# Kernel optimization log

Hardware: AMD Instinct MI355X
Metric: run time of the kernel (lower is better)

Reference implementation:

```python
import jax, jax.numpy as jnp
import numpy as np

B, N, E, T, DIN, H, G, ND, NT, L = 4, 10000, 320000, 16, 16, 64, 64, 16, 3, 7


def _mlp2(x, W1, b1, W2, b2):
    # Linear -> LeakyReLU -> (Dropout: eval identity) -> Linear -> LeakyReLU
    h = jax.nn.leaky_relu(x @ W1 + b1)
    return jax.nn.leaky_relu(h @ W2 + b2)


def _gcn_conv(x, src, dst, ew, nt, W1, b1, W2, b2):
    # x: [B,N,D], nt: [B,N,ND], ew: [*,E,1] broadcastable over batch
    x_in = _mlp2(jnp.concatenate([x, nt], axis=-1), W1, b1, W2, b2)  # [B,N,G]
    msgs = x_in[:, src, :] * ew                                      # gather + weight, [B,E,G]
    aggr = jnp.zeros(x_in.shape, x_in.dtype).at[:, dst, :].add(msgs) # scatter-add, [B,N,G]
    return x + aggr


def _gru(x, Wx, Wh, bx, bh):
    # PyTorch-style GRU over time axis. x: [B,N,T,DIN] -> hs: [T,B,N,H]
    xw = jnp.einsum('bntd,dh->tbnh', x, Wx) + bx  # precompute input projections [T,B,N,3H]
    h0 = jnp.zeros(x.shape[:2] + (Wh.shape[0],), x.dtype)

    def step(h, xw_t):
        hw = h @ Wh + bh
        xr, xz, xn = jnp.split(xw_t, 3, axis=-1)
        hr, hz, hn = jnp.split(hw, 3, axis=-1)
        r = jax.nn.sigmoid(xr + hr)
        z = jax.nn.sigmoid(xz + hz)
        n = jnp.tanh(xn + r * hn)
        h_new = (1 - z) * n + z * h
        return h_new, h_new

    _, hs = jax.lax.scan(step, h0, xw)
    return hs


def reference(input_day, edge_attr, gru_Wx, gru_Wh, gru_bx, gru_bh,
              rnn_fc_W, rnn_fc_b,
              e_emb, e_c0_W1, e_c0_b1, e_c0_W2, e_c0_b2,
              e_c1_W1, e_c1_b1, e_c1_W2, e_c1_b2,
              e_fm_W1, e_fm_b1, e_fm_W2, e_fm_b2,
              g_emb, g_c0_W1, g_c0_b1, g_c0_W2, g_c0_b2,
              g_c1_W1, g_c1_b1, g_c1_W2, g_c1_b2,
              gcn_fc_W, gcn_fc_b,
              edge_index, node_type_ids):
    src, dst = edge_index[0], edge_index[1]

    # KRNN encoder (GRU) + max over time + FC head
    hs = _gru(input_day, gru_Wx, gru_Wh, gru_bx, gru_bh)  # [T,B,N,H]
    rnn_out = hs.max(axis=0)                              # kr_out.max(dim=-2) -> [B,N,H]
    y_rnn = rnn_out @ rnn_fc_W + rnn_fc_b                 # [B,N,L]

    # EdgeNet: GCN stack on static edge_attr, then per-edge pair MLP -> gate
    nt_e = jnp.broadcast_to(e_emb[node_type_ids][None], (B, N, ND))
    ew0 = edge_attr.reshape(1, E, 1)
    x = rnn_out
    x = _gcn_conv(x, src, dst, ew0, nt_e, e_c0_W1, e_c0_b1, e_c0_W2, e_c0_b2)
    x = _gcn_conv(x, src, dst, ew0, nt_e, e_c1_W1, e_c1_b1, e_c1_W2, e_c1_b2)
    edge_x = jnp.concatenate([x[:, src, :], x[:, dst, :]], axis=-1)  # [B,E,2G]
    h = jax.nn.leaky_relu(edge_x @ e_fm_W1 + e_fm_b1)
    edge_gate = jax.nn.relu(h @ e_fm_W2 + e_fm_b2)                   # [B,E,1]

    # Main GCNNet with learned edge gates
    nt_g = jnp.broadcast_to(g_emb[node_type_ids][None], (B, N, ND))
    x = rnn_out
    x = _gcn_conv(x, src, dst, edge_gate, nt_g, g_c0_W1, g_c0_b1, g_c0_W2, g_c0_b2)
    x = _gcn_conv(x, src, dst, edge_gate, nt_g, g_c1_W1, g_c1_b1, g_c1_W2, g_c1_b2)
    y_gcn = x @ gcn_fc_W + gcn_fc_b                                  # [B,N,L]

    return y_rnn + y_gcn


def setup_inputs() -> dict:
    key = jax.random.key(0)
    ks = iter(jax.random.split(key, 48))

    def nrm(shape, s=0.1):
        return jax.random.normal(next(ks), shape, jnp.float32) * s

    inp = {}
    inp['input_day'] = jax.random.normal(next(ks), (B, N, T, DIN), jnp.float32)
    inp['edge_index'] = jax.random.randint(next(ks), (2, E), 0, N)
    inp['node_type_ids'] = jax.random.randint(next(ks), (N,), 0, NT)
    inp['edge_attr'] = jax.random.uniform(next(ks), (E,), jnp.float32)

    inp['gru_Wx'] = nrm((DIN, 3 * H))
    inp['gru_Wh'] = nrm((H, 3 * H))
    inp['gru_bx'] = jnp.zeros((3 * H,), jnp.float32)
    inp['gru_bh'] = jnp.zeros((3 * H,), jnp.float32)
    inp['rnn_fc_W'] = nrm((H, L))
    inp['rnn_fc_b'] = jnp.zeros((L,), jnp.float32)

    inp['e_emb'] = nrm((NT, ND))
    inp['g_emb'] = nrm((NT, ND))
    for pre, in_dim in (('e_c0', H + ND), ('e_c1', G + ND), ('g_c0', H + ND), ('g_c1', G + ND)):
        inp[pre + '_W1'] = nrm((in_dim, G))
        inp[pre + '_b1'] = jnp.zeros((G,), jnp.float32)
        inp[pre + '_W2'] = nrm((G, G))
        inp[pre + '_b2'] = jnp.zeros((G,), jnp.float32)

    inp['e_fm_W1'] = nrm((2 * G, G))
    inp['e_fm_b1'] = jnp.zeros((G,), jnp.float32)
    inp['e_fm_W2'] = nrm((G, 1))
    inp['e_fm_b2'] = jnp.zeros((1,), jnp.float32)

    inp['gcn_fc_W'] = nrm((G, L))
    inp['gcn_fc_b'] = jnp.zeros((L,), jnp.float32)
    return inp
```

## Files before the change

### kernel.cpp

```cpp
#include <hip/hip_runtime.h>
#include <hip/hip_bf16.h>

#define NB 4
#define NN 10000
#define NE 320000
#define BN 40000
#define NL 7

typedef float f32x4 __attribute__((ext_vector_type(4)));
typedef __bf16 bf16x8 __attribute__((ext_vector_type(8)));

__device__ __forceinline__ float bf2f(unsigned short u){
  unsigned x = ((unsigned)u) << 16;
  return __builtin_bit_cast(float, x);
}
__device__ __forceinline__ unsigned short f2bf(float f){
  unsigned u = __builtin_bit_cast(unsigned, f);
  u += 0x7fffu + ((u >> 16) & 1u);
  return (unsigned short)(u >> 16);
}
__device__ __forceinline__ __bf16 f2b(float f){
  return __builtin_bit_cast(__bf16, f2bf(f));
}
__device__ __forceinline__ bf16x8 zero8(){
  uint4 z = make_uint4(0u,0u,0u,0u);
  return __builtin_bit_cast(bf16x8, z);
}
__device__ __forceinline__ bf16x8 one8(){
  uint4 z = make_uint4(0x3f80u,0u,0u,0u);
  return __builtin_bit_cast(bf16x8, z);
}
__device__ __forceinline__ bf16x8 ld8bf(const unsigned short* p){
  uint4 u = *(const uint4*)p;
  return __builtin_bit_cast(bf16x8, u);
}
__device__ __forceinline__ unsigned pk2(float lo, float hi){
  unsigned r;
  asm("v_cvt_pk_bf16_f32 %0, %1, %2" : "=v"(r) : "v"(lo), "v"(hi));
  return r;
}
__device__ __forceinline__ bf16x8 ld8f(const float* p){
  float4 a = *(const float4*)p;
  float4 b = *(const float4*)(p+4);
  uint4 u = make_uint4(pk2(a.x,a.y), pk2(a.z,a.w), pk2(b.x,b.y), pk2(b.z,b.w));
  return __builtin_bit_cast(bf16x8, u);
}
__device__ __forceinline__ float frcp(float x){ return __builtin_amdgcn_rcpf(x); }
__device__ __forceinline__ float sigm(float x){ return frcp(1.f+__expf(-x)); }
__device__ __forceinline__ float tanh_(float x){ return 1.f - 2.f*frcp(__expf(2.f*x)+1.f); }
__device__ __forceinline__ float lrelu(float x){ return x > 0.f ? x : 0.01f*x; }

#define LDS_WAIT() asm volatile("s_waitcnt lgkmcnt(0)" ::: "memory")

__global__ __launch_bounds__(256, 2) void gru_kernel(
    const float* __restrict__ xd,
    const float* __restrict__ Wx,
    const float* __restrict__ Wh,
    const float* __restrict__ bx,
    const float* __restrict__ bh,
    float* __restrict__ rnn)
{
  __shared__ __attribute__((aligned(16))) unsigned short WhT[192][72];
  __shared__ __attribute__((aligned(16))) unsigned short WxT[192][40];
  __shared__ __attribute__((aligned(16))) unsigned short hb[4][16][72];
  int tid = threadIdx.x;
  int wave = tid >> 6, lane = tid & 63;
  int ln16 = lane & 15, quad = lane >> 4;

  for (int i = tid; i < 64*192; i += 256){
    int k = i / 192, n = i - k*192;
    WhT[n][k] = f2bf(Wh[i]);
  }
  for (int i = tid; i < 16*192; i += 256){
    int k = i / 192, n = i - k*192;
    WxT[n][k] = f2bf(Wx[i]);
    WxT[n][17+k] = 0;
  }
  if (tid < 192){
    float bias = (tid < 128) ? (bx[tid] + bh[tid]) : bx[tid];
    WxT[tid][16] = f2bf(bias);
  }
  for (int i = tid; i < 4*16*72; i += 256) ((unsigned short*)hb)[i] = 0;
  __syncthreads();

  int rowbase = blockIdx.x * 64 + wave * 16;

  bf16x8 whf[2][12];
  #pragma unroll
  for (int kt=0; kt<2; ++kt)
    #pragma unroll
    for (int nt=0; nt<12; ++nt)
      whf[kt][nt] = ld8bf(&WhT[nt*16 + ln16][kt*32 + quad*8]);

  f32x4 bhn2[4];
  #pragma unroll
  for (int j=0;j<4;++j)
    bhn2[j] = *(const f32x4*)(bh + 128 + j*16 + quad*4);

  f32x4 hprev[4], vmax[4];
  #pragma unroll
  for (int j=0;j<4;++j){
    hprev[j] = (f32x4){0.f,0.f,0.f,0.f};
    vmax[j]  = (f32x4){-1e30f,-1e30f,-1e30f,-1e30f};
  }

  const float* xrow = xd + (size_t)(rowbase + ln16) * 256;
  unsigned short* hrow = &hb[wave][ln16][0];

  bf16x8 axc;
  if (quad < 2) axc = ld8f(xrow + quad*8);
  else          axc = (quad == 2) ? one8() : zero8();

  for (int t = 0; t < 16; ++t){
    bf16x8 axn;
    if (quad < 2) axn = (t < 15) ? ld8f(xrow + (t+1)*16 + quad*8) : zero8();
    else          axn = (quad == 2) ? one8() : zero8();
    bf16x8 ah0 = ld8bf(hrow + quad*8);
    bf16x8 ah1 = ld8bf(hrow + 32 + quad*8);

    #pragma unroll
    for (int j=0;j<4;++j){
      bf16x8 xr = ld8bf(&WxT[j*16+ln16][quad*8]);
      bf16x8 xz = ld8bf(&WxT[(4+j)*16+ln16][quad*8]);
      bf16x8 xn = ld8bf(&WxT[(8+j)*16+ln16][quad*8]);
      f32x4 z4 = (f32x4){0.f,0.f,0.f,0.f};
      f32x4 ar = __builtin_amdgcn_mfma_f32_16x16x32_bf16(xr, axc, z4, 0,0,0);
      ar = __builtin_amdgcn_mfma_f32_16x16x32_bf16(whf[0][j], ah0, ar, 0,0,0);
      ar = __builtin_amdgcn_mfma_f32_16x16x32_bf16(whf[1][j], ah1, ar, 0,0,0);
      f32x4 az = __builtin_amdgcn_mfma_f32_16x16x32_bf16(xz, axc, z4, 0,0,0);
      az = __builtin_amdgcn_mfma_f32_16x16x32_bf16(whf[0][4+j], ah0, az, 0,0,0);
      az = __builtin_amdgcn_mfma_f32_16x16x32_bf16(whf[1][4+j], ah1, az, 0,0,0);
      f32x4 an = __builtin_amdgcn_mfma_f32_16x16x32_bf16(xn, axc, z4, 0,0,0);
      f32x4 ah = __builtin_amdgcn_mfma_f32_16x16x32_bf16(whf[0][8+j], ah0, bhn2[j], 0,0,0);
      ah = __builtin_amdgcn_mfma_f32_16x16x32_bf16(whf[1][8+j], ah1, ah, 0,0,0);
      f32x4 hv;
      #pragma unroll
      for (int i=0;i<4;++i){
        float r  = sigm(ar[i]);
        float z  = sigm(az[i]);
        float nn = tanh_(an[i] + r * ah[i]);
        float h  = fmaf(z, hprev[j][i]-nn, nn);
        hprev[j][i] = h;
        vmax[j][i] = fmaxf(vmax[j][i], h);
        hv[i] = h;
      }
      *(uint2*)&hb[wave][ln16][j*16+quad*4] = make_uint2(pk2(hv[0],hv[1]), pk2(hv[2],hv[3]));
    }
    LDS_WAIT();
    axc = axn;
  }
  float* orow = rnn + (size_t)(rowbase + ln16)*64;
  #pragma unroll
  for (int j=0;j<4;++j)
    *(f32x4*)(orow + j*16 + quad*4) = vmax[j];
}

__global__ __launch_bounds__(256, 2) void mlp2_kernel(
    const float* __restrict__ x,
    const int* __restrict__ ntid,
    const float* __restrict__ emb,
    const float* __restrict__ W1,
    const float* __restrict__ b1,
    const float* __restrict__ W2,
    const float* __restrict__ b2,
    unsigned short* __restrict__ out)
{
  __shared__ __attribute__((aligned(16))) unsigned short W1T[64][96];
  __shared__ __attribute__((aligned(16))) unsigned short W2T[64][72];
  __shared__ __attribute__((aligned(16))) unsigned short hb[4][16][72];
  __shared__ float sb1[64], sb2[64];
  int tid = threadIdx.x;
  for (int i=tid;i<80*64;i+=256){ int k=i>>6, n=i&63; W1T[n][k]=f2bf(W1[i]); }
  for (int i=tid;i<64*16;i+=256){ int n=i>>4, k=80+(i&15); W1T[n][k]=0; }
  for (int i=tid;i<64*64;i+=256){ int k=i>>6, n=i&63; W2T[n][k]=f2bf(W2[i]); }
  if (tid<64){ sb1[tid]=b1[tid]; sb2[tid]=b2[tid]; }
  __syncthreads();

  int wave = tid>>6, lane = tid&63, ln16 = lane&15, quad = lane>>4;
  int row0 = blockIdx.x*64 + wave*16;
  int r_ = row0 + ln16;
  const float* xr = x + (size_t)r_*64;
  bf16x8 a0 = ld8f(xr + quad*8);
  bf16x8 a1 = ld8f(xr + 32 + quad*8);
  int id = ntid[r_ % NN];
  bf16x8 a2 = (quad<2) ? ld8f(emb + id*16 + quad*8) : zero8();

  f32x4 acc[4];
  #pragma unroll
  for (int nt=0;nt<4;++nt){
    float bb = sb1[nt*16+ln16];
    acc[nt] = (f32x4){bb,bb,bb,bb};
    acc[nt] = __builtin_amdgcn_mfma_f32_16x16x32_bf16(a0, ld8bf(&W1T[nt*16+ln16][quad*8]),    acc[nt], 0,0,0);
    acc[nt] = __builtin_amdgcn_mfma_f32_16x16x32_bf16(a1, ld8bf(&W1T[nt*16+ln16][32+quad*8]), acc[nt], 0,0,0);
    acc[nt] = __builtin_amdgcn_mfma_f32_16x16x32_bf16(a2, ld8bf(&W1T[nt*16+ln16][64+quad*8]), acc[nt], 0,0,0);
  }
  #pragma unroll
  for (int nt=0;nt<4;++nt)
    #pragma unroll
    for (int i=0;i<4;++i)
      hb[wave][quad*4+i][nt*16+ln16] = f2bf(lrelu(acc[nt][i]));
  LDS_WAIT();
  bf16x8 h0 = ld8bf(&hb[wave][ln16][quad*8]);
  bf16x8 h1 = ld8bf(&hb[wave][ln16][32+quad*8]);
  f32x4 acc2[4];
  #pragma unroll
  for (int nt=0;nt<4;++nt){
    float bb = sb2[nt*16+ln16];
    acc2[nt] = (f32x4){bb,bb,bb,bb};
    acc2[nt] = __builtin_amdgcn_mfma_f32_16x16x32_bf16(h0, ld8bf(&W2T[nt*16+ln16][quad*8]),    acc2[nt], 0,0,0);
    acc2[nt] = __builtin_amdgcn_mfma_f32_16x16x32_bf16(h1, ld8bf(&W2T[nt*16+ln16][32+quad*8]), acc2[nt], 0,0,0);
  }
  #pragma unroll
  for (int nt=0;nt<4;++nt)
    #pragma unroll
    for (int i=0;i<4;++i)
      out[(size_t)(row0+quad*4+i)*64 + nt*16+ln16] = f2bf(lrelu(acc2[nt][i]));
}

__global__ __launch_bounds__(256, 2) void uv_kernel(
    const float* __restrict__ x,
    const float* __restrict__ W1,
    unsigned short* __restrict__ uvp)
{
  __shared__ __attribute__((aligned(16))) unsigned short WT[128][72];
  int tid=threadIdx.x;
  for (int i=tid;i<64*64;i+=256){
    int k=i>>6, n=i&63;
    WT[n][k]    = f2bf(W1[i]);
    WT[64+n][k] = f2bf(W1[64*64 + i]);
  }
  __syncthreads();
  int wave=tid>>6, lane=tid&63, ln16=lane&15, quad=lane>>4;
  int row0 = blockIdx.x*64 + wave*16;
  const float* xr = x + (size_t)(row0+ln16)*64;
  bf16x8 a0 = ld8f(xr + quad*8);
  bf16x8 a1 = ld8f(xr + 32 + quad*8);
  f32x4 acc[8];
  #pragma unroll
  for (int nt=0;nt<8;++nt){
    acc[nt] = (f32x4){0.f,0.f,0.f,0.f};
    acc[nt] = __builtin_amdgcn_mfma_f32_16x16x32_bf16(a0, ld8bf(&WT[nt*16+ln16][quad*8]),    acc[nt], 0,0,0);
    acc[nt] = __builtin_amdgcn_mfma_f32_16x16x32_bf16(a1, ld8bf(&WT[nt*16+ln16][32+quad*8]), acc[nt], 0,0,0);
  }
  #pragma unroll
  for (int nt=0;nt<8;++nt)
    #pragma unroll
    for (int i=0;i<4;++i)
      uvp[(size_t)(row0+quad*4+i)*128 + nt*16+ln16] = f2bf(acc[nt][i]);
}

__global__ __launch_bounds__(256) void count_kernel(const int* __restrict__ ei, int* __restrict__ counts){
  int e = blockIdx.x*256+threadIdx.x;
  atomicAdd(&counts[ei[NE+e]], 1);
}
__global__ __launch_bounds__(1024) void scan_kernel(const int* __restrict__ counts,
                                                    int* __restrict__ rowptr, int* __restrict__ cursor){
  __shared__ int incl[10240];
  __shared__ int wsum[16];
  int tid=threadIdx.x, wave=tid>>6, lane=tid&63;
  int base = wave*640;
  int carry=0;
  #pragma unroll
  for (int c=0;c<10;++c){
    int i = base + c*64 + lane;
    int v = (i<NN)? counts[i] : 0;
    int s = v;
    #pragma unroll
    for (int off=1;off<64;off<<=1){
      int t_ = __shfl_up(s, off);
      if (lane>=off) s += t_;
    }
    s += carry;
    incl[base + c*64 + lane] = s;
    carry = __shfl(s, 63);
  }
  if (lane==63) wsum[wave]=carry;
  __syncthreads();
  if (wave==0){
    int w_ = (lane<16)? wsum[lane]:0;
    #pragma unroll
    for (int off=1;off<16;off<<=1){
      int t_ = __shfl_up(w_, off);
      if (lane>=off) w_ += t_;
    }
    if (lane<16) wsum[lane]=w_;
  }
  __syncthreads();
  int woff = (wave>0)? wsum[wave-1] : 0;
  #pragma unroll
  for (int c=0;c<10;++c){
    int i = base + c*64 + lane;
    if (i<NN){
      int excl = incl[i] + woff - counts[i];
      rowptr[i]=excl; cursor[i]=excl;
    }
  }
  if (tid==0) rowptr[NN]=wsum[15];
}
__global__ __launch_bounds__(256) void fill_kernel(const int* __restrict__ ei,
                                                   const float* __restrict__ ea,
                                                   int* __restrict__ cursor,
                                                   int* __restrict__ ssrc,
                                                   float* __restrict__ wcsr){
  int e = blockIdx.x*256+threadIdx.x;
  int d = ei[NE+e];
  int pos = atomicAdd(&cursor[d],1);
  ssrc[pos]=ei[e];
  wcsr[pos]=ea[e];
}

__global__ __launch_bounds__(256) void aggr_kernel(
    const float* x,
    const unsigned short* __restrict__ xin,
    const int* __restrict__ rowptr,
    const int* __restrict__ ssrc,
    const float* __restrict__ wp,
    int bstride,
    float* out)
{
  int tid=threadIdx.x;
  int wave=tid>>6, lane=tid&63;
  int sub=lane>>4, l=lane&15;
  int bid = blockIdx.x*4 + wave;
  int b = bid / NN, n = bid - b*NN;
  int p0 = rowptr[n], p1 = rowptr[n+1];
  const unsigned short* xb_ = xin + (size_t)b*NN*64;
  const float* wb = wp + (size_t)b*bstride;
  float a0=0.f, a1=0.f, a2=0.f, a3=0.f;
  #pragma unroll 4
  for (int p=p0+sub; p<p1; p+=4){
    int s = ssrc[p];
    float w = wb[p];
    uint2 m = *(const uint2*)(xb_ + (size_t)s*64 + l*4);
    a0 += bf2f((unsigned short)(m.x & 0xffffu)) * w;
    a1 += bf2f((unsigned short)(m.x >> 16)) * w;
    a2 += bf2f((unsigned short)(m.y & 0xffffu)) * w;
    a3 += bf2f((unsigned short)(m.y >> 16)) * w;
  }
  a0 += __shfl_xor(a0,16); a0 += __shfl_xor(a0,32);
  a1 += __shfl_xor(a1,16); a1 += __shfl_xor(a1,32);
  a2 += __shfl_xor(a2,16); a2 += __shfl_xor(a2,32);
  a3 += __shfl_xor(a3,16); a3 += __shfl_xor(a3,32);
  if (sub==0){
    float4 base = *(const float4*)(x + (size_t)bid*64 + l*4);
    float4 o; o.x=base.x+a0; o.y=base.y+a1; o.z=base.z+a2; o.w=base.w+a3;
    *(float4*)(out + (size_t)bid*64 + l*4) = o;
  }
}

__global__ __launch_bounds__(256) void aggr_final_kernel(
    const float* x,
    const unsigned short* __restrict__ xin,
    const int* __restrict__ rowptr,
    const int* __restrict__ ssrc,
    const float* __restrict__ wp,
    const float* __restrict__ rnn,
    const float* __restrict__ Wr, const float* __restrict__ br,
    const float* __restrict__ Wg, const float* __restrict__ bg,
    float* __restrict__ out)
{
  __shared__ float sWr[448], sWg[448], sb[7];
  int tid=threadIdx.x;
  for (int i=tid;i<448;i+=256){ sWr[i]=Wr[i]; sWg[i]=Wg[i]; }
  if (tid<7) sb[tid]=br[tid]+bg[tid];
  __syncthreads();
  int wave=tid>>6, lane=tid&63;
  int sub=lane>>4, l=lane&15;
  int bid = blockIdx.x*4 + wave;
  int b = bid / NN, n = bid - b*NN;
  int p0 = rowptr[n], p1 = rowptr[n+1];
  const unsigned short* xb_ = xin + (size_t)b*NN*64;
  const float* wb = wp + (size_t)b*NE;
  float a0=0.f, a1=0.f, a2=0.f, a3=0.f;
  #pragma unroll 4
  for (int p=p0+sub; p<p1; p+=4){
    int s = ssrc[p];
    float w = wb[p];
    uint2 m = *(const uint2*)(xb_ + (size_t)s*64 + l*4);
    a0 += bf2f((unsigned short)(m.x & 0xffffu)) * w;
    a1 += bf2f((unsigned short)(m.x >> 16)) * w;
    a2 += bf2f((unsigned short)(m.y & 0xffffu)) * w;
    a3 += bf2f((unsigned short)(m.y >> 16)) * w;
  }
  a0 += __shfl_xor(a0,16); a0 += __shfl_xor(a0,32);
  a1 += __shfl_xor(a1,16); a1 += __shfl_xor(a1,32);
  a2 += __shfl_xor(a2,16); a2 += __shfl_xor(a2,32);
  a3 += __shfl_xor(a3,16); a3 += __shfl_xor(a3,32);
  if (sub==0){
    float4 base = *(const float4*)(x + (size_t)bid*64 + l*4);
    float o0=base.x+a0, o1=base.y+a1, o2=base.z+a2, o3=base.w+a3;
    float4 rr = *(const float4*)(rnn + (size_t)bid*64 + l*4);
    float part[7];
    #pragma unroll
    for (int q=0;q<7;++q)
      part[q] = o0*sWg[(l*4+0)*7+q] + o1*sWg[(l*4+1)*7+q]
              + o2*sWg[(l*4+2)*7+q] + o3*sWg[(l*4+3)*7+q]
              + rr.x*sWr[(l*4+0)*7+q] + rr.y*sWr[(l*4+1)*7+q]
              + rr.z*sWr[(l*4+2)*7+q] + rr.w*sWr[(l*4+3)*7+q];
    #pragma unroll
    for (int q=0;q<7;++q){
      part[q] += __shfl_xor(part[q],1);
      part[q] += __shfl_xor(part[q],2);
      part[q] += __shfl_xor(part[q],4);
      part[q] += __shfl_xor(part[q],8);
    }
    if (l==0){
      #pragma unroll
      for (int q=0;q<7;++q) out[(size_t)bid*7+q] = part[q] + sb[q];
    }
  }
}

__global__ __launch_bounds__(256) void gate_kernel(
    const unsigned short* __restrict__ uvp,
    const int* __restrict__ rowptr,
    const int* __restrict__ ssrc,
    const float* __restrict__ b1,
    const float* __restrict__ W2,
    const float* __restrict__ b2,
    float* __restrict__ gate)
{
  int tid=threadIdx.x;
  int wave=tid>>6, lane=tid&63;
  int sub=lane>>4, l=lane&15;
  int bid = blockIdx.x*4 + wave;
  int b = bid / NN, n = bid - b*NN;
  int p0 = rowptr[n], p1 = rowptr[n+1];
  const unsigned short* ub = uvp + (size_t)b*NN*128;
  uint2 vu = *(const uint2*)(ub + (size_t)n*128 + 64 + l*4);
  float v0=bf2f((unsigned short)(vu.x&0xffffu)), v1=bf2f((unsigned short)(vu.x>>16));
  float v2=bf2f((unsigned short)(vu.y&0xffffu)), v3=bf2f((unsigned short)(vu.y>>16));
  float4 bb = *(const float4*)(b1 + l*4);
  float4 ww = *(const float4*)(W2 + l*4);
  float b2v = b2[0];
  float* gb = gate + (size_t)b*NE;
  #pragma unroll 4
  for (int p=p0+sub; p<p1; p+=4){
    int s = ssrc[p];
    uint2 uu = *(const uint2*)(ub + (size_t)s*128 + l*4);
    float h0 = lrelu(bf2f((unsigned short)(uu.x&0xffffu)) + v0 + bb.x);
    float h1 = lrelu(bf2f((unsigned short)(uu.x>>16))     + v1 + bb.y);
    float h2 = lrelu(bf2f((unsigned short)(uu.y&0xffffu)) + v2 + bb.z);
    float h3 = lrelu(bf2f((unsigned short)(uu.y>>16))     + v3 + bb.w);
    float part = h0*ww.x + h1*ww.y + h2*ww.z + h3*ww.w;
    part += __shfl_xor(part,1);
    part += __shfl_xor(part,2);
    part += __shfl_xor(part,4);
    part += __shfl_xor(part,8);
    if (l==0){
      float g = part + b2v;
      gb[p] = g>0.f ? g : 0.f;
    }
  }
}

extern "C" void kernel_launch(void* const* d_in, const int* in_sizes, int n_in,
                              void* d_out, int out_size, void* d_ws, size_t ws_size,
                              hipStream_t stream)
{
  (void)in_sizes; (void)n_in; (void)out_size; (void)ws_size;
  const float* input_day = (const float*)d_in[0];
  const int* ei    = (const int*)d_in[1];
  const int* ntid  = (const int*)d_in[2];
  const float* edge_attr = (const float*)d_in[3];
  const float* gWx = (const float*)d_in[4];
  const float* gWh = (const float*)d_in[5];
  const float* gbx = (const float*)d_in[6];
  const float* gbh = (const float*)d_in[7];
  const float* rW  = (const float*)d_in[8];
  const float* rb  = (const float*)d_in[9];
  const float* eemb= (const float*)d_in[10];
  const float* gemb= (const float*)d_in[11];
  const float* ec0W1=(const float*)d_in[12];
  const float* ec0b1=(const float*)d_in[13];
  const float* ec0W2=(const float*)d_in[14];
  const float* ec0b2=(const float*)d_in[15];
  const float* ec1W1=(const float*)d_in[16];
  const float* ec1b1=(const float*)d_in[17];
  const float* ec1W2=(const float*)d_in[18];
  const float* ec1b2=(const float*)d_in[19];
  const float* gc0W1=(const float*)d_in[20];
  const float* gc0b1=(const float*)d_in[21];
  const float* gc0W2=(const float*)d_in[22];
  const float* gc0b2=(const float*)d_in[23];
  const float* gc1W1=(const float*)d_in[24];
  const float* gc1b1=(const float*)d_in[25];
  const float* gc1W2=(const float*)d_in[26];
  const float* gc1b2=(const float*)d_in[27];
  const float* efmW1=(const float*)d_in[28];
  const float* efmb1=(const float*)d_in[29];
  const float* efmW2=(const float*)d_in[30];
  const float* efmb2=(const float*)d_in[31];
  const float* gcnW =(const float*)d_in[32];
  const float* gcnb =(const float*)d_in[33];

  char* ws = (char*)d_ws;
  float*          rnn = (float*)(ws);
  float*          xe  = (float*)(ws + 10240000);
  unsigned short* xin = (unsigned short*)(ws + 20480000);
  unsigned short* uvp = (unsigned short*)(ws + 25600000);
  float*          gat = (float*)(ws + 35840000);
  int* rowptr= (int*)(ws + 40960000);
  int* cursor= (int*)(ws + 41000064);
  int* counts= (int*)(ws + 41040064);
  int*   ssrc= (int*)(ws + 41080064);
  float* wcsr= (float*)(ws + 42360064);

  hipMemsetAsync(counts, 0, NN*sizeof(int), stream);
  count_kernel<<<NE/256, 256, 0, stream>>>(ei, counts);
  scan_kernel<<<1, 1024, 0, stream>>>(counts, rowptr, cursor);
  fill_kernel<<<NE/256, 256, 0, stream>>>(ei, edge_attr, cursor, ssrc, wcsr);

  gru_kernel<<<625, 256, 0, stream>>>(input_day, gWx, gWh, gbx, gbh, rnn);

  mlp2_kernel<<<625, 256, 0, stream>>>(rnn, ntid, eemb, ec0W1, ec0b1, ec0W2, ec0b2, xin);
  aggr_kernel<<<BN/4, 256, 0, stream>>>(rnn, xin, rowptr, ssrc, wcsr, 0, xe);
  mlp2_kernel<<<625, 256, 0, stream>>>(xe, ntid, eemb, ec1W1, ec1b1, ec1W2, ec1b2, xin);
  aggr_kernel<<<BN/4, 256, 0, stream>>>(xe, xin, rowptr, ssrc, wcsr, 0, xe);

  uv_kernel<<<625, 256, 0, stream>>>(xe, efmW1, uvp);
  gate_kernel<<<BN/4, 256, 0, stream>>>(uvp, rowptr, ssrc, efmb1, efmW2, efmb2, gat);

  mlp2_kernel<<<625, 256, 0, stream>>>(rnn, ntid, gemb, gc0W1, gc0b1, gc0W2, gc0b2, xin);
  aggr_kernel<<<BN/4, 256, 0, stream>>>(rnn, xin, rowptr, ssrc, gat, NE, xe);
  mlp2_kernel<<<625, 256, 0, stream>>>(xe, ntid, gemb, gc1W1, gc1b1, gc1W2, gc1b2, xin);
  aggr_final_kernel<<<BN/4, 256, 0, stream>>>(xe, xin, rowptr, ssrc, gat, rnn,
                                              rW, rb, gcnW, gcnb, (float*)d_out);
}
```

Before: 462.0 us.

## Permute GRU gate columns so hidden state stays in registers across timesteps

```diff
diff --git a/kernel.cpp b/kernel.cpp
--- a/kernel.cpp
+++ b/kernel.cpp
@@ -52,7 +52,7 @@
 
 #define LDS_WAIT() asm volatile("s_waitcnt lgkmcnt(0)" ::: "memory")
 
-__global__ __launch_bounds__(256, 2) void gru_kernel(
+__global__ __launch_bounds__(256, 3) void gru_kernel(
     const float* __restrict__ xd,
     const float* __restrict__ Wx,
     const float* __restrict__ Wh,
@@ -62,25 +62,30 @@
 {
   __shared__ __attribute__((aligned(16))) unsigned short WhT[192][72];
   __shared__ __attribute__((aligned(16))) unsigned short WxT[192][40];
-  __shared__ __attribute__((aligned(16))) unsigned short hb[4][16][72];
   int tid = threadIdx.x;
   int wave = tid >> 6, lane = tid & 63;
   int ln16 = lane & 15, quad = lane >> 4;
 
   for (int i = tid; i < 64*192; i += 256){
-    int k = i / 192, n = i - k*192;
-    WhT[n][k] = f2bf(Wh[i]);
+    int k = i / 192, p = i - k*192;
+    int j = (p>>4)&3, m = p&15;
+    int d = (p & 0xC0) | ((j&1)<<5) | ((m>>2)<<3) | ((j>>1)<<2) | (m&3);
+    WhT[p][k] = f2bf(Wh[k*192 + d]);
   }
   for (int i = tid; i < 16*192; i += 256){
-    int k = i / 192, n = i - k*192;
-    WxT[n][k] = f2bf(Wx[i]);
-    WxT[n][17+k] = 0;
+    int k = i / 192, p = i - k*192;
+    int j = (p>>4)&3, m = p&15;
+    int d = (p & 0xC0) | ((j&1)<<5) | ((m>>2)<<3) | ((j>>1)<<2) | (m&3);
+    WxT[p][k] = f2bf(Wx[k*192 + d]);
+    WxT[p][17+k] = 0;
   }
   if (tid < 192){
-    float bias = (tid < 128) ? (bx[tid] + bh[tid]) : bx[tid];
-    WxT[tid][16] = f2bf(bias);
-  }
-  for (int i = tid; i < 4*16*72; i += 256) ((unsigned short*)hb)[i] = 0;
+    int p = tid;
+    int j = (p>>4)&3, m = p&15;
+    int d = (p & 0xC0) | ((j&1)<<5) | ((m>>2)<<3) | ((j>>1)<<2) | (m&3);
+    float bias = (d < 128) ? (bx[d] + bh[d]) : bx[d];
+    WxT[p][16] = f2bf(bias);
+  }
   __syncthreads();
 
   int rowbase = blockIdx.x * 64 + wave * 16;
@@ -95,17 +100,18 @@
   f32x4 bhn2[4];
   #pragma unroll
   for (int j=0;j<4;++j)
-    bhn2[j] = *(const f32x4*)(bh + 128 + j*16 + quad*4);
+    bhn2[j] = *(const f32x4*)(bh + 128 + ((j&1)<<5) + quad*8 + ((j>>1)<<2));
 
   f32x4 hprev[4], vmax[4];
+  uint2 hpk[4];
   #pragma unroll
   for (int j=0;j<4;++j){
     hprev[j] = (f32x4){0.f,0.f,0.f,0.f};
     vmax[j]  = (f32x4){-1e30f,-1e30f,-1e30f,-1e30f};
+    hpk[j]   = make_uint2(0u,0u);
   }
 
   const float* xrow = xd + (size_t)(rowbase + ln16) * 256;
-  unsigned short* hrow = &hb[wave][ln16][0];
 
   bf16x8 axc;
   if (quad < 2) axc = ld8f(xrow + quad*8);
@@ -115,8 +121,10 @@
     bf16x8 axn;
     if (quad < 2) axn = (t < 15) ? ld8f(xrow + (t+1)*16 + quad*8) : zero8();
     else          axn = (quad == 2) ? one8() : zero8();
-    bf16x8 ah0 = ld8bf(hrow + quad*8);
-    bf16x8 ah1 = ld8bf(hrow + 32 + quad*8);
+    uint4 u0 = make_uint4(hpk[0].x, hpk[0].y, hpk[2].x, hpk[2].y);
+    uint4 u1 = make_uint4(hpk[1].x, hpk[1].y, hpk[3].x, hpk[3].y);
+    bf16x8 ah0 = __builtin_bit_cast(bf16x8, u0);
+    bf16x8 ah1 = __builtin_bit_cast(bf16x8, u1);
 
     #pragma unroll
     for (int j=0;j<4;++j){
@@ -144,15 +152,14 @@
         vmax[j][i] = fmaxf(vmax[j][i], h);
         hv[i] = h;
       }
-      *(uint2*)&hb[wave][ln16][j*16+quad*4] = make_uint2(pk2(hv[0],hv[1]), pk2(hv[2],hv[3]));
-    }
-    LDS_WAIT();
+      hpk[j] = make_uint2(pk2(hv[0],hv[1]), pk2(hv[2],hv[3]));
+    }
     axc = axn;
   }
   float* orow = rnn + (size_t)(rowbase + ln16)*64;
   #pragma unroll
   for (int j=0;j<4;++j)
-    *(f32x4*)(orow + j*16 + quad*4) = vmax[j];
+    *(f32x4*)(orow + ((j&1)<<5) + quad*8 + ((j>>1)<<2)) = vmax[j];
 }
 
 __global__ __launch_bounds__(256, 2) void mlp2_kernel(
```

Result: slower. 535.9 us (+16.0%).
